# Optimization experiments

Hardware: AMD Instinct MI355X
Metric: run time of the kernel (lower is better)

## Reference

```python
import jax, jax.numpy as jnp
import numpy as np


def _gcn_norm(edge_index, num_nodes, dtype):
    # PyG GCNConv.norm: add self-loops (weight 1), symmetric deg^{-1/2} normalization
    row, col = edge_index[0], edge_index[1]
    loop = jnp.arange(num_nodes, dtype=row.dtype)
    row = jnp.concatenate([row, loop])
    col = jnp.concatenate([col, loop])
    ew = jnp.ones(row.shape[0], dtype=dtype)
    deg = jax.ops.segment_sum(ew, row, num_segments=num_nodes)
    dis = jnp.where(deg > 0, jax.lax.rsqrt(deg), 0.0)
    norm = dis[row] * ew * dis[col]
    return row, col, norm


def _masked_gcn_conv(x, row, col, norm, sigma, W, b, num_nodes):
    # mask_features: edge gather -> diff/sigma -> square -> scatter-add -> exp mask
    h = (x[col] - x[row]) / sigma            # [E, F]
    h = norm[:, None] * h * h                # [E, F]
    mask = jax.ops.segment_sum(h, row, num_segments=num_nodes)        # [N, F]
    deg = jax.ops.segment_sum(jnp.ones_like(norm), row, num_segments=num_nodes)  # degree(source), >=1 due to self-loops
    x = x * jnp.exp(-mask / deg[:, None])
    # GCNConv: linear transform then normalized aggregation source->target
    xw = x @ W                               # [N, O]
    out = jax.ops.segment_sum(norm[:, None] * xw[row], col, num_segments=num_nodes)
    return out + b


def setup_inputs() -> dict:
    key = jax.random.key(0)
    ks = jax.random.split(key, 8)
    N, E, F, H, C = 100000, 1600000, 128, 64, 40
    g = 1.414  # xavier gain used for sigma
    return {
        "x": jax.random.normal(ks[0], (N, F), jnp.float32),
        "edge_index": jax.random.randint(ks[1], (2, E), 0, N, jnp.int64),
        "sigma1": jax.random.uniform(ks[2], (1, F), jnp.float32, -1.0, 1.0) * (g * np.sqrt(6.0 / (1 + F))),
        "W1": jax.random.normal(ks[3], (F, H), jnp.float32) * (1.0 / np.sqrt(F)),
        "b1": jnp.zeros((H,), jnp.float32),
        "sigma2": jax.random.uniform(ks[4], (1, H), jnp.float32, -1.0, 1.0) * (g * np.sqrt(6.0 / (1 + H))),
        "W2": jax.random.normal(ks[5], (H, C), jnp.float32) * (1.0 / np.sqrt(H)),
        "b2": jnp.zeros((C,), jnp.float32),
    }


def reference(x, edge_index, sigma1, W1, b1, sigma2, W2, b2):
    N = x.shape[0]
    row, col, norm = _gcn_norm(edge_index, N, x.dtype)
    x = _masked_gcn_conv(x, row, col, norm, sigma1, W1, b1, N)
    x = jax.nn.relu(x)
    # dropout is identity in eval mode
    x = _masked_gcn_conv(x, row, col, norm, sigma2, W2, b2, N)
    return jax.nn.log_softmax(x, axis=1)
```

## Files before the change

### kernel.cpp

```cpp
#include <hip/hip_runtime.h>
#include <cmath>

constexpr int F1 = 128;
constexpr int H  = 64;
constexpr int NC = 40;
constexpr int NXCD = 8;

constexpr int SCAN_TPB = 256;
constexpr int SCAN_IPT = 8;
constexpr int SCAN_EPB = SCAN_TPB * SCAN_IPT;

__device__ inline unsigned short f2bf(float f) {
    union { float f; unsigned u; } v; v.f = f;
    return (unsigned short)((v.u + 0x7FFFu + ((v.u >> 16) & 1u)) >> 16);
}
__device__ inline float bflo(unsigned p) { union { float f; unsigned u; } v; v.u = p << 16; return v.f; }
__device__ inline float bfhi(unsigned p) { union { float f; unsigned u; } v; v.u = p & 0xFFFF0000u; return v.f; }
__device__ inline void unpack8(uint4 raw, float* d) {
    d[0] = bflo(raw.x); d[1] = bfhi(raw.x); d[2] = bflo(raw.y); d[3] = bfhi(raw.y);
    d[4] = bflo(raw.z); d[5] = bfhi(raw.z); d[6] = bflo(raw.w); d[7] = bfhi(raw.w);
}

__global__ void isg_kernel(const float* __restrict__ s1, float* __restrict__ i1,
                           const float* __restrict__ s2, float* __restrict__ i2) {
    int i = threadIdx.x;
    if (i < F1) i1[i] = 1.0f / s1[i];
    if (i < H)  i2[i] = 1.0f / s2[i];
}

__global__ void prep_u_kernel(const float* __restrict__ x, const float* __restrict__ isg,
                              unsigned short* __restrict__ u, size_t n8, int F) {
    size_t idx = (size_t)blockIdx.x * blockDim.x + threadIdx.x;
    if (idx >= n8) return;
    size_t base = idx * 8;
    int fk = (int)(base % (size_t)F);
    float4 a0 = *(const float4*)&x[base];
    float4 a1 = *(const float4*)&x[base + 4];
    float4 s0 = *(const float4*)&isg[fk];
    float4 s1 = *(const float4*)&isg[fk + 4];
    uint4 p;
    p.x = (unsigned)f2bf(a0.x * s0.x) | ((unsigned)f2bf(a0.y * s0.y) << 16);
    p.y = (unsigned)f2bf(a0.z * s0.z) | ((unsigned)f2bf(a0.w * s0.w) << 16);
    p.z = (unsigned)f2bf(a1.x * s1.x) | ((unsigned)f2bf(a1.y * s1.y) << 16);
    p.w = (unsigned)f2bf(a1.z * s1.z) | ((unsigned)f2bf(a1.w * s1.w) << 16);
    *(uint4*)&u[base] = p;
}

__global__ void count8_kernel(const int* __restrict__ row, const int* __restrict__ col,
                              int* __restrict__ cntO, int* __restrict__ cntI,
                              int E, int chunk, int stride) {
    int p = blockIdx.x & (NXCD - 1);
    int gid = blockIdx.x >> 3;
    unsigned lo = (unsigned)(p * chunk);
    for (int e = gid * blockDim.x + threadIdx.x; e < E; e += stride) {
        int r = row[e], c = col[e];
        if ((unsigned)r - lo < (unsigned)chunk) atomicAdd(&cntO[r], 1);
        if ((unsigned)c - lo < (unsigned)chunk) atomicAdd(&cntI[c], 1);
    }
}

__global__ void scan_partial_kernel(const int* __restrict__ cnt, int* __restrict__ bsum, int M) {
    __shared__ int red[SCAN_TPB];
    int t = threadIdx.x;
    int i0 = blockIdx.x * SCAN_EPB + t * SCAN_IPT;
    int s = 0;
#pragma unroll
    for (int k = 0; k < SCAN_IPT; ++k) {
        int i = i0 + k;
        if (i < M) s += cnt[i];
    }
    red[t] = s;
    __syncthreads();
    for (int off = SCAN_TPB / 2; off > 0; off >>= 1) {
        if (t < off) red[t] += red[t + off];
        __syncthreads();
    }
    if (t == 0) bsum[blockIdx.x] = red[0];
}

__global__ void scan_offsets_kernel(int* __restrict__ bsum, int nb,
                                    int* __restrict__ rowptrO, int* __restrict__ rowptrI,
                                    int N, int E) {
    __shared__ int sh[1024];
    int t = threadIdx.x;
    sh[t] = (t < nb) ? bsum[t] : 0;
    __syncthreads();
    for (int off = 1; off < 1024; off <<= 1) {
        int v = (t >= off) ? sh[t - off] : 0;
        __syncthreads();
        sh[t] += v;
        __syncthreads();
    }
    if (t < nb) bsum[t] = (t > 0) ? sh[t - 1] : 0;
    if (t == 0) { rowptrO[N] = E; rowptrI[N] = E; }
}

__global__ void scan_final_kernel(int* __restrict__ cntO, int* __restrict__ cntI,
                                  const int* __restrict__ bsum,
                                  int* __restrict__ rowptrO, int* __restrict__ rowptrI,
                                  float* __restrict__ dis, int N, int E) {
    __shared__ int sh[SCAN_TPB];
    int t = threadIdx.x;
    int M = 2 * N;
    const int* cnt = cntO;
    int i0 = blockIdx.x * SCAN_EPB + t * SCAN_IPT;
    int cv[SCAN_IPT], pre[SCAN_IPT];
    int run = 0;
#pragma unroll
    for (int k = 0; k < SCAN_IPT; ++k) {
        int i = i0 + k;
        cv[k] = (i < M) ? cnt[i] : 0;
        pre[k] = run;
        run += cv[k];
    }
    sh[t] = run;
    __syncthreads();
    for (int off = 1; off < SCAN_TPB; off <<= 1) {
        int v = (t >= off) ? sh[t - off] : 0;
        __syncthreads();
        sh[t] += v;
        __syncthreads();
    }
    int toff = ((t > 0) ? sh[t - 1] : 0) + bsum[blockIdx.x];
#pragma unroll
    for (int k = 0; k < SCAN_IPT; ++k) {
        int i = i0 + k;
        if (i < M) {
            int val = toff + pre[k];
            if (i < N) {
                rowptrO[i] = val;
                cntO[i] = val;
                dis[i] = rsqrtf((float)(cv[k] + 1));
            } else {
                rowptrI[i - N] = val - E;
                cntI[i - N] = val - E;
            }
        }
    }
}

__global__ void build8_kernel(const int* __restrict__ row, const int* __restrict__ col,
                              int* __restrict__ curO, int* __restrict__ curI,
                              int* __restrict__ adjO, int* __restrict__ adjI,
                              int E, int chunk, int stride) {
    int p = blockIdx.x & (NXCD - 1);
    int gid = blockIdx.x >> 3;
    unsigned lo = (unsigned)(p * chunk);
    for (int e = gid * blockDim.x + threadIdx.x; e < E; e += stride) {
        int r = row[e], c = col[e];
        if ((unsigned)r - lo < (unsigned)chunk) adjO[atomicAdd(&curO[r], 1)] = c;
        if ((unsigned)c - lo < (unsigned)chunk) adjI[atomicAdd(&curI[c], 1)] = r;
    }
}

template<int F, int O, int R>
__global__ void fused_mask_gemm_kernel(const int* __restrict__ rowptr, const int* __restrict__ adj,
                                       const float* __restrict__ dis, const float* __restrict__ x,
                                       const unsigned short* __restrict__ u,
                                       const float* __restrict__ W,
                                       unsigned short* __restrict__ Ybf, int N) {
    constexpr int NT = R * 64;
    constexpr int G = F / 8;
    constexpr int NPI = 64 / G;
    __shared__ __align__(16) float Ws[F * O];
    __shared__ __align__(16) float Xs[R][F];
    int tid = threadIdx.x;
    for (int i = tid; i < F * O; i += NT) Ws[i] = W[i];
    int w = tid >> 6, lane = tid & 63;
    int h = lane / G, j = lane % G;
    int r = blockIdx.x * R + w;
    if (r < N) {
        int beg = rowptr[r], end = rowptr[r + 1];
        float dr = dis[r];
        float inv_deg = 1.0f / (float)(end - beg + 1);
        float ur[8], acc[8];
        unpack8(*(const uint4*)&u[(size_t)r * F + 8 * j], ur);
#pragma unroll
        for (int k = 0; k < 8; ++k) acc[k] = 0.0f;
        for (int t = beg; t < end; t += 2 * NPI) {
            int e0 = t + h, e1 = t + NPI + h;
            int c0 = adj[min(e0, end - 1)];
            int c1 = adj[min(e1, end - 1)];
            float d0 = (e0 < end) ? dis[c0] : 0.0f;
            float d1 = (e1 < end) ? dis[c1] : 0.0f;
            uint4 rw0 = *(const uint4*)&u[(size_t)c0 * F + 8 * j];
            uint4 rw1 = *(const uint4*)&u[(size_t)c1 * F + 8 * j];
            float n0 = dr * d0, n1 = dr * d1;
            float uc[8];
            unpack8(rw0, uc);
#pragma unroll
            for (int q = 0; q < 8; ++q) {
                float d = uc[q] - ur[q];
                acc[q] = fmaf(n0 * d, d, acc[q]);
            }
            unpack8(rw1, uc);
#pragma unroll
            for (int q = 0; q < 8; ++q) {
                float d = uc[q] - ur[q];
                acc[q] = fmaf(n1 * d, d, acc[q]);
            }
        }
#pragma unroll
        for (int off = G; off < 64; off <<= 1) {
#pragma unroll
            for (int k = 0; k < 8; ++k) acc[k] += __shfl_xor(acc[k], off);
        }
        if (h == 0) {
            float4 a0 = *(const float4*)&x[(size_t)r * F + 8 * j];
            float4 a1 = *(const float4*)&x[(size_t)r * F + 8 * j + 4];
            float xm[8] = {a0.x, a0.y, a0.z, a0.w, a1.x, a1.y, a1.z, a1.w};
#pragma unroll
            for (int k = 0; k < 8; ++k) xm[k] *= expf(-acc[k] * inv_deg);
            *(float4*)&Xs[w][8 * j]     = make_float4(xm[0], xm[1], xm[2], xm[3]);
            *(float4*)&Xs[w][8 * j + 4] = make_float4(xm[4], xm[5], xm[6], xm[7]);
        }
    }
    __syncthreads();
    if (r < N && lane < O) {
        float acc = 0.0f;
#pragma unroll
        for (int fq = 0; fq < F / 4; ++fq) {
            float4 xs = *(const float4*)&Xs[w][4 * fq];
            acc = fmaf(xs.x, Ws[(4 * fq + 0) * O + lane], acc);
            acc = fmaf(xs.y, Ws[(4 * fq + 1) * O + lane], acc);
            acc = fmaf(xs.z, Ws[(4 * fq + 2) * O + lane], acc);
            acc = fmaf(xs.w, Ws[(4 * fq + 3) * O + lane], acc);
        }
        float other = __shfl_xor(acc, 1);
        if (!(lane & 1)) {
            *(unsigned*)&Ybf[(size_t)r * O + lane] =
                (unsigned)f2bf(acc) | ((unsigned)f2bf(other) << 16);
        }
    }
}

__global__ void agg_relu_kernel(const int* __restrict__ rowptr, const int* __restrict__ adj,
                                const float* __restrict__ dis, const unsigned short* __restrict__ ybf,
                                const float* __restrict__ bias, float* __restrict__ h1,
                                unsigned short* __restrict__ u2, const float* __restrict__ isg2, int N) {
    int c = blockIdx.x * (blockDim.x >> 6) + (threadIdx.x >> 6);
    if (c >= N) return;
    int lane = threadIdx.x & 63;
    int h = lane >> 3, j = lane & 7;
    int beg = rowptr[c], end = rowptr[c + 1];
    float dc = dis[c];
    float acc[8];
#pragma unroll
    for (int k = 0; k < 8; ++k) acc[k] = 0.0f;
    for (int t = beg; t < end; t += 16) {
        int e0 = t + h, e1 = t + 8 + h;
        int c0 = adj[min(e0, end - 1)];
        int c1 = adj[min(e1, end - 1)];
        float d0 = (e0 < end) ? dis[c0] : 0.0f;
        float d1 = (e1 < end) ? dis[c1] : 0.0f;
        uint4 rw0 = *(const uint4*)&ybf[(size_t)c0 * H + 8 * j];
        uint4 rw1 = *(const uint4*)&ybf[(size_t)c1 * H + 8 * j];
        float n0 = dc * d0, n1 = dc * d1;
        float v[8];
        unpack8(rw0, v);
#pragma unroll
        for (int q = 0; q < 8; ++q) acc[q] = fmaf(n0, v[q], acc[q]);
        unpack8(rw1, v);
#pragma unroll
        for (int q = 0; q < 8; ++q) acc[q] = fmaf(n1, v[q], acc[q]);
    }
#pragma unroll
    for (int off = 8; off < 64; off <<= 1) {
#pragma unroll
        for (int k = 0; k < 8; ++k) acc[k] += __shfl_xor(acc[k], off);
    }
    if (h == 0) {
        float sv[8];
        unpack8(*(const uint4*)&ybf[(size_t)c * H + 8 * j], sv);
        float4 b0 = *(const float4*)&bias[8 * j];
        float4 b1v = *(const float4*)&bias[8 * j + 4];
        float bb[8] = {b0.x, b0.y, b0.z, b0.w, b1v.x, b1v.y, b1v.z, b1v.w};
        float4 s0 = *(const float4*)&isg2[8 * j];
        float4 s1 = *(const float4*)&isg2[8 * j + 4];
        float sg[8] = {s0.x, s0.y, s0.z, s0.w, s1.x, s1.y, s1.z, s1.w};
        float hv[8];
        float d2 = dc * dc;
#pragma unroll
        for (int k = 0; k < 8; ++k) hv[k] = fmaxf(fmaf(d2, sv[k], acc[k]) + bb[k], 0.0f);
        *(float4*)&h1[(size_t)c * H + 8 * j]     = make_float4(hv[0], hv[1], hv[2], hv[3]);
        *(float4*)&h1[(size_t)c * H + 8 * j + 4] = make_float4(hv[4], hv[5], hv[6], hv[7]);
        uint4 p;
        p.x = (unsigned)f2bf(hv[0] * sg[0]) | ((unsigned)f2bf(hv[1] * sg[1]) << 16);
        p.y = (unsigned)f2bf(hv[2] * sg[2]) | ((unsigned)f2bf(hv[3] * sg[3]) << 16);
        p.z = (unsigned)f2bf(hv[4] * sg[4]) | ((unsigned)f2bf(hv[5] * sg[5]) << 16);
        p.w = (unsigned)f2bf(hv[6] * sg[6]) | ((unsigned)f2bf(hv[7] * sg[7]) << 16);
        *(uint4*)&u2[(size_t)c * H + 8 * j] = p;
    }
}

__global__ void agg_lsm_kernel(const int* __restrict__ rowptr, const int* __restrict__ adj,
                               const float* __restrict__ dis, const unsigned short* __restrict__ ybf,
                               const float* __restrict__ bias, float* __restrict__ out, int N) {
    int c = blockIdx.x * (blockDim.x >> 6) + (threadIdx.x >> 6);
    if (c >= N) return;
    int lane = threadIdx.x & 63;
    int h = lane >> 4, j = lane & 15;
    bool active = j < 10;
    int beg = rowptr[c], end = rowptr[c + 1];
    float dc = dis[c];
    float a[4] = {0.f, 0.f, 0.f, 0.f};
    for (int t = beg; t < end; t += 8) {
        int e0 = t + h, e1 = t + 4 + h;
        int c0 = adj[min(e0, end - 1)];
        int c1 = adj[min(e1, end - 1)];
        float d0 = (e0 < end) ? dis[c0] : 0.0f;
        float d1 = (e1 < end) ? dis[c1] : 0.0f;
        uint2 rw0 = active ? *(const uint2*)&ybf[(size_t)c0 * NC + 4 * j] : make_uint2(0u, 0u);
        uint2 rw1 = active ? *(const uint2*)&ybf[(size_t)c1 * NC + 4 * j] : make_uint2(0u, 0u);
        float n0 = dc * d0, n1 = dc * d1;
        a[0] = fmaf(n0, bflo(rw0.x), a[0]); a[1] = fmaf(n0, bfhi(rw0.x), a[1]);
        a[2] = fmaf(n0, bflo(rw0.y), a[2]); a[3] = fmaf(n0, bfhi(rw0.y), a[3]);
        a[0] = fmaf(n1, bflo(rw1.x), a[0]); a[1] = fmaf(n1, bfhi(rw1.x), a[1]);
        a[2] = fmaf(n1, bflo(rw1.y), a[2]); a[3] = fmaf(n1, bfhi(rw1.y), a[3]);
    }
#pragma unroll
    for (int off = 16; off < 64; off <<= 1) {
#pragma unroll
        for (int k = 0; k < 4; ++k) a[k] += __shfl_xor(a[k], off);
    }
    bool wr = (h == 0) && active;
    float v[4] = {-INFINITY, -INFINITY, -INFINITY, -INFINITY};
    if (wr) {
        uint2 sr = *(const uint2*)&ybf[(size_t)c * NC + 4 * j];
        float sv[4] = {bflo(sr.x), bfhi(sr.x), bflo(sr.y), bfhi(sr.y)};
        float4 bb = *(const float4*)&bias[4 * j];
        float b4[4] = {bb.x, bb.y, bb.z, bb.w};
        float d2 = dc * dc;
#pragma unroll
        for (int k = 0; k < 4; ++k) v[k] = fmaf(d2, sv[k], a[k]) + b4[k];
    }
    float m = fmaxf(fmaxf(v[0], v[1]), fmaxf(v[2], v[3]));
#pragma unroll
    for (int off = 8; off > 0; off >>= 1) m = fmaxf(m, __shfl_xor(m, off));
    float s = wr ? (expf(v[0] - m) + expf(v[1] - m) + expf(v[2] - m) + expf(v[3] - m)) : 0.0f;
#pragma unroll
    for (int off = 8; off > 0; off >>= 1) s += __shfl_xor(s, off);
    float mls = m + logf(s);
    if (wr)
        *(float4*)&out[(size_t)c * NC + 4 * j] = make_float4(v[0] - mls, v[1] - mls, v[2] - mls, v[3] - mls);
}

extern "C" void kernel_launch(void* const* d_in, const int* in_sizes, int n_in,
                              void* d_out, int out_size, void* d_ws, size_t ws_size,
                              hipStream_t stream) {
    const float* x    = (const float*)d_in[0];
    const int*   ei   = (const int*)  d_in[1];
    const float* sig1 = (const float*)d_in[2];
    const float* W1   = (const float*)d_in[3];
    const float* b1   = (const float*)d_in[4];
    const float* sig2 = (const float*)d_in[5];
    const float* W2   = (const float*)d_in[6];
    const float* b2   = (const float*)d_in[7];
    float* out = (float*)d_out;

    const int N = in_sizes[0] / F1;
    const int E = in_sizes[1] / 2;
    const int* row = ei;
    const int* col = ei + E;

    char* w = (char*)d_ws;
    auto alloc = [&](size_t bytes) { void* q = w; w += (bytes + 255) & ~255ull; return q; };
    int*   cntO    = (int*)  alloc((size_t)2 * N * 4);
    int*   cntI    = cntO + N;
    int*   rowptrO = (int*)  alloc((size_t)(N + 1) * 4);
    int*   rowptrI = (int*)  alloc((size_t)(N + 1) * 4);
    int*   adjO    = (int*)  alloc((size_t)E * 4);
    int*   adjI    = (int*)  alloc((size_t)E * 4);
    float* dis     = (float*)alloc((size_t)N * 4);
    float* isg1    = (float*)alloc(F1 * 4);
    float* isg2    = (float*)alloc(H * 4);
    int*   bsum    = (int*)  alloc(1024 * 4);
    unsigned short* u1   = (unsigned short*)alloc((size_t)N * F1 * 2);
    unsigned short* u2   = (unsigned short*)alloc((size_t)N * H * 2);
    unsigned short* ybf1 = (unsigned short*)alloc((size_t)N * H * 2);
    float* h1      = (float*)alloc((size_t)N * H * 4);
    unsigned short* ybf2 = u1;

    const int B = 256;
    const int chunk = (N + NXCD - 1) / NXCD;
    const int WPP = 1024;
    const int stride8 = WPP * B;
    dim3 g8(NXCD * WPP);
    const int M = 2 * N;
    const int nb = (M + SCAN_EPB - 1) / SCAN_EPB;

    hipMemsetAsync(cntO, 0, (size_t)2 * N * 4, stream);
    isg_kernel<<<1, 128, 0, stream>>>(sig1, isg1, sig2, isg2);
    prep_u_kernel<<<(int)(((size_t)N * F1 / 8 + B - 1) / B), B, 0, stream>>>(x, isg1, u1, (size_t)N * F1 / 8, F1);
    count8_kernel<<<g8, B, 0, stream>>>(row, col, cntO, cntI, E, chunk, stride8);
    scan_partial_kernel<<<nb, SCAN_TPB, 0, stream>>>(cntO, bsum, M);
    scan_offsets_kernel<<<1, 1024, 0, stream>>>(bsum, nb, rowptrO, rowptrI, N, E);
    scan_final_kernel<<<nb, SCAN_TPB, 0, stream>>>(cntO, cntI, bsum, rowptrO, rowptrI, dis, N, E);
    build8_kernel<<<g8, B, 0, stream>>>(row, col, cntO, cntI, adjO, adjI, E, chunk, stride8);

    fused_mask_gemm_kernel<F1, H, 8><<<(N + 7) / 8, 512, 0, stream>>>(rowptrO, adjO, dis, x, u1, W1, ybf1, N);
    agg_relu_kernel<<<(N + 3) / 4, B, 0, stream>>>(rowptrI, adjI, dis, ybf1, b1, h1, u2, isg2, N);

    fused_mask_gemm_kernel<H, NC, 8><<<(N + 7) / 8, 512, 0, stream>>>(rowptrO, adjO, dis, h1, u2, W2, ybf2, N);
    agg_lsm_kernel<<<(N + 3) / 4, B, 0, stream>>>(rowptrI, adjI, dis, ybf2, b2, out, N);
}
```

Baseline: 657.1 us.

## Store precomputed edge norms alongside CSR neighbors and merge prep into count kernel

The CSR adjacency arrays become (neighbor, norm) int2 pairs, with the symmetric norm dis[r]*dis[c] computed once during the build. This removes the random per-edge dis[] gathers from all four aggregation kernels. In exchange the adjacency traffic doubles and the build does extra dis loads. Separately, the bf16 prep of x is folded into the edge-count launch as extra blocks, which saves one launch and lets the two independent jobs overlap.

```diff
diff --git a/kernel.cpp b/kernel.cpp
--- a/kernel.cpp
+++ b/kernel.cpp
@@ -28,34 +28,36 @@
     if (i < H)  i2[i] = 1.0f / s2[i];
 }
 
-__global__ void prep_u_kernel(const float* __restrict__ x, const float* __restrict__ isg,
-                              unsigned short* __restrict__ u, size_t n8, int F) {
-    size_t idx = (size_t)blockIdx.x * blockDim.x + threadIdx.x;
-    if (idx >= n8) return;
-    size_t base = idx * 8;
-    int fk = (int)(base % (size_t)F);
-    float4 a0 = *(const float4*)&x[base];
-    float4 a1 = *(const float4*)&x[base + 4];
-    float4 s0 = *(const float4*)&isg[fk];
-    float4 s1 = *(const float4*)&isg[fk + 4];
-    uint4 p;
-    p.x = (unsigned)f2bf(a0.x * s0.x) | ((unsigned)f2bf(a0.y * s0.y) << 16);
-    p.y = (unsigned)f2bf(a0.z * s0.z) | ((unsigned)f2bf(a0.w * s0.w) << 16);
-    p.z = (unsigned)f2bf(a1.x * s1.x) | ((unsigned)f2bf(a1.y * s1.y) << 16);
-    p.w = (unsigned)f2bf(a1.z * s1.z) | ((unsigned)f2bf(a1.w * s1.w) << 16);
-    *(uint4*)&u[base] = p;
-}
-
-__global__ void count8_kernel(const int* __restrict__ row, const int* __restrict__ col,
-                              int* __restrict__ cntO, int* __restrict__ cntI,
-                              int E, int chunk, int stride) {
-    int p = blockIdx.x & (NXCD - 1);
-    int gid = blockIdx.x >> 3;
-    unsigned lo = (unsigned)(p * chunk);
-    for (int e = gid * blockDim.x + threadIdx.x; e < E; e += stride) {
-        int r = row[e], c = col[e];
-        if ((unsigned)r - lo < (unsigned)chunk) atomicAdd(&cntO[r], 1);
-        if ((unsigned)c - lo < (unsigned)chunk) atomicAdd(&cntI[c], 1);
+__global__ void count8_prep_kernel(const int* __restrict__ row, const int* __restrict__ col,
+                                   int* __restrict__ cntO, int* __restrict__ cntI,
+                                   int E, int chunk, int stride, int cntBlocks,
+                                   const float* __restrict__ x, const float* __restrict__ isg,
+                                   unsigned short* __restrict__ u, size_t n8) {
+    int bid = blockIdx.x;
+    if (bid < cntBlocks) {
+        int p = bid & (NXCD - 1);
+        int gid = bid >> 3;
+        unsigned lo = (unsigned)(p * chunk);
+        for (int e = gid * blockDim.x + threadIdx.x; e < E; e += stride) {
+            int r = row[e], c = col[e];
+            if ((unsigned)r - lo < (unsigned)chunk) atomicAdd(&cntO[r], 1);
+            if ((unsigned)c - lo < (unsigned)chunk) atomicAdd(&cntI[c], 1);
+        }
+    } else {
+        size_t idx = (size_t)(bid - cntBlocks) * blockDim.x + threadIdx.x;
+        if (idx >= n8) return;
+        size_t base = idx * 8;
+        int fk = (int)(base % (size_t)F1);
+        float4 a0 = *(const float4*)&x[base];
+        float4 a1 = *(const float4*)&x[base + 4];
+        float4 s0 = *(const float4*)&isg[fk];
+        float4 s1 = *(const float4*)&isg[fk + 4];
+        uint4 p4;
+        p4.x = (unsigned)f2bf(a0.x * s0.x) | ((unsigned)f2bf(a0.y * s0.y) << 16);
+        p4.y = (unsigned)f2bf(a0.z * s0.z) | ((unsigned)f2bf(a0.w * s0.w) << 16);
+        p4.z = (unsigned)f2bf(a1.x * s1.x) | ((unsigned)f2bf(a1.y * s1.y) << 16);
+        p4.w = (unsigned)f2bf(a1.z * s1.z) | ((unsigned)f2bf(a1.w * s1.w) << 16);
+        *(uint4*)&u[base] = p4;
     }
 }
 
@@ -141,21 +143,28 @@
 
 __global__ void build8_kernel(const int* __restrict__ row, const int* __restrict__ col,
                               int* __restrict__ curO, int* __restrict__ curI,
-                              int* __restrict__ adjO, int* __restrict__ adjI,
+                              int2* __restrict__ adjO2, int2* __restrict__ adjI2,
+                              const float* __restrict__ dis,
                               int E, int chunk, int stride) {
     int p = blockIdx.x & (NXCD - 1);
     int gid = blockIdx.x >> 3;
     unsigned lo = (unsigned)(p * chunk);
     for (int e = gid * blockDim.x + threadIdx.x; e < E; e += stride) {
         int r = row[e], c = col[e];
-        if ((unsigned)r - lo < (unsigned)chunk) adjO[atomicAdd(&curO[r], 1)] = c;
-        if ((unsigned)c - lo < (unsigned)chunk) adjI[atomicAdd(&curI[c], 1)] = r;
+        bool inR = (unsigned)r - lo < (unsigned)chunk;
+        bool inC = (unsigned)c - lo < (unsigned)chunk;
+        if (inR | inC) {
+            float nrm = dis[r] * dis[c];
+            int nb = __float_as_int(nrm);
+            if (inR) adjO2[atomicAdd(&curO[r], 1)] = make_int2(c, nb);
+            if (inC) adjI2[atomicAdd(&curI[c], 1)] = make_int2(r, nb);
+        }
     }
 }
 
 template<int F, int O, int R>
-__global__ void fused_mask_gemm_kernel(const int* __restrict__ rowptr, const int* __restrict__ adj,
-                                       const float* __restrict__ dis, const float* __restrict__ x,
+__global__ void fused_mask_gemm_kernel(const int* __restrict__ rowptr, const int2* __restrict__ adj2,
+                                       const float* __restrict__ x,
                                        const unsigned short* __restrict__ u,
                                        const float* __restrict__ W,
                                        unsigned short* __restrict__ Ybf, int N) {
@@ -171,7 +180,6 @@
     int r = blockIdx.x * R + w;
     if (r < N) {
         int beg = rowptr[r], end = rowptr[r + 1];
-        float dr = dis[r];
         float inv_deg = 1.0f / (float)(end - beg + 1);
         float ur[8], acc[8];
         unpack8(*(const uint4*)&u[(size_t)r * F + 8 * j], ur);
@@ -179,13 +187,12 @@
         for (int k = 0; k < 8; ++k) acc[k] = 0.0f;
         for (int t = beg; t < end; t += 2 * NPI) {
             int e0 = t + h, e1 = t + NPI + h;
-            int c0 = adj[min(e0, end - 1)];
-            int c1 = adj[min(e1, end - 1)];
-            float d0 = (e0 < end) ? dis[c0] : 0.0f;
-            float d1 = (e1 < end) ? dis[c1] : 0.0f;
-            uint4 rw0 = *(const uint4*)&u[(size_t)c0 * F + 8 * j];
-            uint4 rw1 = *(const uint4*)&u[(size_t)c1 * F + 8 * j];
-            float n0 = dr * d0, n1 = dr * d1;
+            int2 a0 = adj2[min(e0, end - 1)];
+            int2 a1 = adj2[min(e1, end - 1)];
+            float n0 = (e0 < end) ? __int_as_float(a0.y) : 0.0f;
+            float n1 = (e1 < end) ? __int_as_float(a1.y) : 0.0f;
+            uint4 rw0 = *(const uint4*)&u[(size_t)a0.x * F + 8 * j];
+            uint4 rw1 = *(const uint4*)&u[(size_t)a1.x * F + 8 * j];
             float uc[8];
             unpack8(rw0, uc);
 #pragma unroll
@@ -234,7 +241,7 @@
     }
 }
 
-__global__ void agg_relu_kernel(const int* __restrict__ rowptr, const int* __restrict__ adj,
+__global__ void agg_relu_kernel(const int* __restrict__ rowptr, const int2* __restrict__ adj2,
                                 const float* __restrict__ dis, const unsigned short* __restrict__ ybf,
                                 const float* __restrict__ bias, float* __restrict__ h1,
                                 unsigned short* __restrict__ u2, const float* __restrict__ isg2, int N) {
@@ -243,19 +250,17 @@
     int lane = threadIdx.x & 63;
     int h = lane >> 3, j = lane & 7;
     int beg = rowptr[c], end = rowptr[c + 1];
-    float dc = dis[c];
     float acc[8];
 #pragma unroll
     for (int k = 0; k < 8; ++k) acc[k] = 0.0f;
     for (int t = beg; t < end; t += 16) {
         int e0 = t + h, e1 = t + 8 + h;
-        int c0 = adj[min(e0, end - 1)];
-        int c1 = adj[min(e1, end - 1)];
-        float d0 = (e0 < end) ? dis[c0] : 0.0f;
-        float d1 = (e1 < end) ? dis[c1] : 0.0f;
-        uint4 rw0 = *(const uint4*)&ybf[(size_t)c0 * H + 8 * j];
-        uint4 rw1 = *(const uint4*)&ybf[(size_t)c1 * H + 8 * j];
-        float n0 = dc * d0, n1 = dc * d1;
+        int2 a0 = adj2[min(e0, end - 1)];
+        int2 a1 = adj2[min(e1, end - 1)];
+        float n0 = (e0 < end) ? __int_as_float(a0.y) : 0.0f;
+        float n1 = (e1 < end) ? __int_as_float(a1.y) : 0.0f;
+        uint4 rw0 = *(const uint4*)&ybf[(size_t)a0.x * H + 8 * j];
+        uint4 rw1 = *(const uint4*)&ybf[(size_t)a1.x * H + 8 * j];
         float v[8];
         unpack8(rw0, v);
 #pragma unroll
@@ -270,6 +275,7 @@
         for (int k = 0; k < 8; ++k) acc[k] += __shfl_xor(acc[k], off);
     }
     if (h == 0) {
+        float dc = dis[c];
         float sv[8];
         unpack8(*(const uint4*)&ybf[(size_t)c * H + 8 * j], sv);
         float4 b0 = *(const float4*)&bias[8 * j];
@@ -293,7 +299,7 @@
     }
 }
 
-__global__ void agg_lsm_kernel(const int* __restrict__ rowptr, const int* __restrict__ adj,
+__global__ void agg_lsm_kernel(const int* __restrict__ rowptr, const int2* __restrict__ adj2,
                                const float* __restrict__ dis, const unsigned short* __restrict__ ybf,
                                const float* __restrict__ bias, float* __restrict__ out, int N) {
     int c = blockIdx.x * (blockDim.x >> 6) + (threadIdx.x >> 6);
@@ -302,17 +308,15 @@
     int h = lane >> 4, j = lane & 15;
     bool active = j < 10;
     int beg = rowptr[c], end = rowptr[c + 1];
-    float dc = dis[c];
     float a[4] = {0.f, 0.f, 0.f, 0.f};
     for (int t = beg; t < end; t += 8) {
         int e0 = t + h, e1 = t + 4 + h;
-        int c0 = adj[min(e0, end - 1)];
-        int c1 = adj[min(e1, end - 1)];
-        float d0 = (e0 < end) ? dis[c0] : 0.0f;
-        float d1 = (e1 < end) ? dis[c1] : 0.0f;
-        uint2 rw0 = active ? *(const uint2*)&ybf[(size_t)c0 * NC + 4 * j] : make_uint2(0u, 0u);
-        uint2 rw1 = active ? *(const uint2*)&ybf[(size_t)c1 * NC + 4 * j] : make_uint2(0u, 0u);
-        float n0 = dc * d0, n1 = dc * d1;
+        int2 a0 = adj2[min(e0, end - 1)];
+        int2 a1 = adj2[min(e1, end - 1)];
+        float n0 = (e0 < end) ? __int_as_float(a0.y) : 0.0f;
+        float n1 = (e1 < end) ? __int_as_float(a1.y) : 0.0f;
+        uint2 rw0 = active ? *(const uint2*)&ybf[(size_t)a0.x * NC + 4 * j] : make_uint2(0u, 0u);
+        uint2 rw1 = active ? *(const uint2*)&ybf[(size_t)a1.x * NC + 4 * j] : make_uint2(0u, 0u);
         a[0] = fmaf(n0, bflo(rw0.x), a[0]); a[1] = fmaf(n0, bfhi(rw0.x), a[1]);
         a[2] = fmaf(n0, bflo(rw0.y), a[2]); a[3] = fmaf(n0, bfhi(rw0.y), a[3]);
         a[0] = fmaf(n1, bflo(rw1.x), a[0]); a[1] = fmaf(n1, bfhi(rw1.x), a[1]);
@@ -326,6 +330,7 @@
     bool wr = (h == 0) && active;
     float v[4] = {-INFINITY, -INFINITY, -INFINITY, -INFINITY};
     if (wr) {
+        float dc = dis[c];
         uint2 sr = *(const uint2*)&ybf[(size_t)c * NC + 4 * j];
         float sv[4] = {bflo(sr.x), bfhi(sr.x), bflo(sr.y), bfhi(sr.y)};
         float4 bb = *(const float4*)&bias[4 * j];
@@ -369,8 +374,8 @@
     int*   cntI    = cntO + N;
     int*   rowptrO = (int*)  alloc((size_t)(N + 1) * 4);
     int*   rowptrI = (int*)  alloc((size_t)(N + 1) * 4);
-    int*   adjO    = (int*)  alloc((size_t)E * 4);
-    int*   adjI    = (int*)  alloc((size_t)E * 4);
+    int2*  adjO2   = (int2*) alloc((size_t)E * 8);
+    int2*  adjI2   = (int2*) alloc((size_t)E * 8);
     float* dis     = (float*)alloc((size_t)N * 4);
     float* isg1    = (float*)alloc(F1 * 4);
     float* isg2    = (float*)alloc(H * 4);
@@ -385,22 +390,24 @@
     const int chunk = (N + NXCD - 1) / NXCD;
     const int WPP = 1024;
     const int stride8 = WPP * B;
-    dim3 g8(NXCD * WPP);
+    const int cntBlocks = NXCD * WPP;
+    const size_t n8 = (size_t)N * F1 / 8;
+    const int prepBlocks = (int)((n8 + B - 1) / B);
     const int M = 2 * N;
     const int nb = (M + SCAN_EPB - 1) / SCAN_EPB;
 
     hipMemsetAsync(cntO, 0, (size_t)2 * N * 4, stream);
     isg_kernel<<<1, 128, 0, stream>>>(sig1, isg1, sig2, isg2);
-    prep_u_kernel<<<(int)(((size_t)N * F1 / 8 + B - 1) / B), B, 0, stream>>>(x, isg1, u1, (size_t)N * F1 / 8, F1);
-    count8_kernel<<<g8, B, 0, stream>>>(row, col, cntO, cntI, E, chunk, stride8);
+    count8_prep_kernel<<<cntBlocks + prepBlocks, B, 0, stream>>>(
+        row, col, cntO, cntI, E, chunk, stride8, cntBlocks, x, isg1, u1, n8);
     scan_partial_kernel<<<nb, SCAN_TPB, 0, stream>>>(cntO, bsum, M);
     scan_offsets_kernel<<<1, 1024, 0, stream>>>(bsum, nb, rowptrO, rowptrI, N, E);
     scan_final_kernel<<<nb, SCAN_TPB, 0, stream>>>(cntO, cntI, bsum, rowptrO, rowptrI, dis, N, E);
-    build8_kernel<<<g8, B, 0, stream>>>(row, col, cntO, cntI, adjO, adjI, E, chunk, stride8);
-
-    fused_mask_gemm_kernel<F1, H, 8><<<(N + 7) / 8, 512, 0, stream>>>(rowptrO, adjO, dis, x, u1, W1, ybf1, N);
-    agg_relu_kernel<<<(N + 3) / 4, B, 0, stream>>>(rowptrI, adjI, dis, ybf1, b1, h1, u2, isg2, N);
-
-    fused_mask_gemm_kernel<H, NC, 8><<<(N + 7) / 8, 512, 0, stream>>>(rowptrO, adjO, dis, h1, u2, W2, ybf2, N);
-    agg_lsm_kernel<<<(N + 3) / 4, B, 0, stream>>>(rowptrI, adjI, dis, ybf2, b2, out, N);
-}
+    build8_kernel<<<cntBlocks, B, 0, stream>>>(row, col, cntO, cntI, adjO2, adjI2, dis, E, chunk, stride8);
+
+    fused_mask_gemm_kernel<F1, H, 8><<<(N + 7) / 8, 512, 0, stream>>>(rowptrO, adjO2, x, u1, W1, ybf1, N);
+    agg_relu_kernel<<<(N + 3) / 4, B, 0, stream>>>(rowptrI, adjI2, dis, ybf1, b1, h1, u2, isg2, N);
+
+    fused_mask_gemm_kernel<H, NC, 8><<<(N + 7) / 8, 512, 0, stream>>>(rowptrO, adjO2, h1, u2, W2, ybf2, N);
+    agg_lsm_kernel<<<(N + 3) / 4, B, 0, stream>>>(rowptrI, adjI2, dis, ybf2, b2, out, N);
+}
```

Result: faster. 632.7 us (-3.7%).
